# Optimization experiments

Hardware: AMD Instinct MI355X
Metric: run time of the kernel (lower is better)

Reference implementation:

```python
import jax, jax.numpy as jnp
import numpy as np

DIM = 1024
DIM_HEAD = 64
INNER = 1024
HEADS = INNER // DIM_HEAD  # 16
QNUM = 64
MULT = 4
SCALE = DIM_HEAD ** -0.5
EPS = 1e-5


def setup_inputs() -> dict:
    key = jax.random.key(0)
    ks = jax.random.split(key, 9)
    S, B, N = 8, 128, 32
    x = jax.random.normal(ks[0], (S, B, N, DIM), dtype=jnp.float32)
    mask = jax.random.randint(ks[1], (S, B, 1), 0, 2, dtype=jnp.int32)
    q = jax.random.normal(ks[2], (QNUM, INNER), dtype=jnp.float32)
    W_kv = jax.random.normal(ks[3], (DIM, 2 * INNER), dtype=jnp.float32) * 0.02
    ln_g = jnp.ones((INNER,), dtype=jnp.float32)
    ln_b = jnp.zeros((INNER,), dtype=jnp.float32)
    W1 = jax.random.normal(ks[4], (INNER, INNER * MULT * 2), dtype=jnp.float32) * 0.02
    b1 = jnp.zeros((INNER * MULT * 2,), dtype=jnp.float32)
    W2 = jax.random.normal(ks[5], (INNER * MULT, INNER), dtype=jnp.float32) * 0.02
    b2 = jnp.zeros((INNER,), dtype=jnp.float32)
    return {"x": x, "mask": mask, "q": q, "W_kv": W_kv, "ln_g": ln_g,
            "ln_b": ln_b, "W1": W1, "b1": b1, "W2": W2, "b2": b2}


def reference(x, mask, q, W_kv, ln_g, ln_b, W1, b1, W2, b2):
    # x: (S, B, N, D) -> (S, N, B, D); attention keys run over original B axis
    x = jnp.transpose(x, (0, 2, 1, 3))
    S, N, B, _ = x.shape
    kv = x @ W_kv                                  # (S, N, B, 2*INNER)
    k, v = jnp.split(kv, 2, axis=-1)
    # split heads: (S, N, B, I) -> (S, N, H, B, Dh)
    k = k.reshape(S, N, B, HEADS, DIM_HEAD).transpose(0, 1, 3, 2, 4)
    v = v.reshape(S, N, B, HEADS, DIM_HEAD).transpose(0, 1, 3, 2, 4)
    qh = q.reshape(QNUM, HEADS, DIM_HEAD).transpose(1, 0, 2)  # (H, Q, Dh)
    sim = jnp.einsum('hqd,snhjd->snhqj', qh, k) * SCALE        # (S,N,H,Q,B)
    # mask: (S, B, J); rearrange 's i j->s j i' then [:,0,:] == mask[:, :, 0]
    m = mask[:, :, 0][:, None, None, None, :]                  # (S,1,1,1,B)
    sim = jnp.where(m == 0, jnp.float32(-1e10), sim)
    attn = jax.nn.softmax(sim, axis=-1)
    out = jnp.einsum('snhqj,snhjd->snhqd', attn, v)            # (S,N,H,Q,Dh)
    out = out.transpose(0, 1, 3, 2, 4).reshape(S, N, QNUM, INNER)
    # PreNorm(Residual(FeedForward)): y = LN(out); return FF(y) + y
    mu = jnp.mean(out, axis=-1, keepdims=True)
    var = jnp.var(out, axis=-1, keepdims=True)
    y = (out - mu) * jax.lax.rsqrt(var + EPS) * ln_g + ln_b
    u = y @ W1 + b1
    a, g = jnp.split(u, 2, axis=-1)
    ff = (a * jax.nn.gelu(g, approximate=False)) @ W2 + b2
    return ff + y
```

## Files before the change

### kernel.cpp

```cpp
#include <hip/hip_runtime.h>
#include <stdint.h>
#include <math.h>

#define SCALE  0.125f

typedef __bf16 bf16;
typedef __bf16 bf16x8 __attribute__((ext_vector_type(8)));
typedef float  f32x4  __attribute__((ext_vector_type(4)));
typedef float  f32x16 __attribute__((ext_vector_type(16)));

__device__ __forceinline__ ushort f2b(float f) {
  union { float f; uint32_t u; } v; v.f = f;
  uint32_t u = v.u;
  return (ushort)((u + 0x7fffu + ((u >> 16) & 1u)) >> 16);
}
__device__ __forceinline__ float b2f(ushort s) {
  union { uint32_t u; float f; } v; v.u = ((uint32_t)s) << 16;
  return v.f;
}
__device__ __forceinline__ void g2l16(const ushort* g, ushort* l) {
  __builtin_amdgcn_global_load_lds(
      (const __attribute__((address_space(1))) void*)g,
      (__attribute__((address_space(3))) void*)l, 16, 0, 0);
}
__device__ __forceinline__ float erf_fast(float x) {
  float ax = fabsf(x);
  float t  = __builtin_amdgcn_rcpf(1.0f + 0.3275911f * ax);
  float p  = t * (0.254829592f + t * (-0.284496736f + t * (1.421413741f +
             t * (-1.453152027f + t * 1.061405429f))));
  float e  = __expf(-ax * ax);
  float r  = 1.0f - p * e;
  return copysignf(r, x);
}

__global__ __launch_bounds__(256) void conv_x_kernel(const float* __restrict__ x,
                                                     ushort* __restrict__ xb) {
  int idx = blockIdx.x * 256 + threadIdx.x;
  int d4 = idx & 255;
  int n  = (idx >> 8) & 31;
  int b  = (idx >> 13) & 127;
  int s  = idx >> 20;
  float4 v = *(const float4*)(x + (size_t)(((s*128 + b)*32 + n) << 10) + (d4 << 2));
  ushort4 o;
  o.x = f2b(v.x); o.y = f2b(v.y); o.z = f2b(v.z); o.w = f2b(v.w);
  *(ushort4*)(xb + (size_t)(((s*32 + n)*128 + b) << 10) + (d4 << 2)) = o;
}

__global__ __launch_bounds__(256) void conv_q_kernel(const float* __restrict__ q,
                                                     ushort* __restrict__ qb) {
  int idx = blockIdx.x * 256 + threadIdx.x;
  float4 v = *(const float4*)(q + (size_t)idx * 4);
  ushort4 o;
  o.x = f2b(v.x); o.y = f2b(v.y); o.z = f2b(v.z); o.w = f2b(v.w);
  *(ushort4*)(qb + (size_t)idx * 4) = o;
}

__global__ __launch_bounds__(256) void transpose_w_kernel(const float* __restrict__ W,
                                                          ushort* __restrict__ Wt,
                                                          int K, int N, int mode) {
  __shared__ float tile[32][33];
  int rt = blockIdx.x, kt = blockIdx.y;
  int r0 = rt * 32;
  int tx = threadIdx.x & 31, ty = threadIdx.x >> 5;
  int src;
  if (mode == 1) {
    int rp = r0 + tx;
    int g6 = rp >> 6, w = rp & 63;
    src = (w < 32) ? (g6*32 + w) : (4096 + g6*32 + (w - 32));
  } else {
    src = r0 + tx;
  }
  for (int i = ty; i < 32; i += 8)
    tile[i][tx] = W[(size_t)(kt*32 + i) * N + src];
  __syncthreads();
  for (int i = ty; i < 32; i += 8)
    Wt[(size_t)(r0 + i) * K + kt*32 + tx] = f2b(tile[tx][i]);
}

template <int EPI, int K, int NCOLS>
__global__ __launch_bounds__(256, 4) void gemm_bt(const ushort* __restrict__ A,
                                                  const ushort* __restrict__ Bt,
                                                  float* __restrict__ outf,
                                                  ushort* __restrict__ outb,
                                                  const float* __restrict__ bias,
                                                  const float* __restrict__ resid) {
  __shared__ ushort As[128 * 64];
  __shared__ ushort Bs[128 * 64];
  constexpr int nBn = NCOLS >> 7;
  const int bm = blockIdx.x / nBn, bn = blockIdx.x % nBn;
  const int t = threadIdx.x;
  const int wave = t >> 6, lane = t & 63;
  const int c32 = lane & 31, hi = lane >> 5;
  const int wm = ((wave >> 1) << 6), wn = ((wave & 1) << 6);
  const int swz = c32 & 7;

  const int srow = wave*8 + (lane >> 3);
  const int skg  = (lane & 7) ^ ((lane >> 3) & 7);
  const ushort* ag = A  + (size_t)(bm*128 + srow) * K + skg*8;
  const ushort* bg = Bt + (size_t)(bn*128 + srow) * K + skg*8;
  ushort* asl = As + wave * 512;
  ushort* bsl = Bs + wave * 512;

  f32x16 acc[2][2] = {};

#pragma unroll 2
  for (int k0 = 0; k0 < K; k0 += 64) {
#pragma unroll
    for (int c = 0; c < 4; c++) {
      g2l16(ag + (size_t)c*32*K + k0, asl + c*2048);
      g2l16(bg + (size_t)c*32*K + k0, bsl + c*2048);
    }
    __syncthreads();
#pragma unroll
    for (int kb = 0; kb < 2; kb++) {
      bf16x8 af[2][2], bfr[2][2];
#pragma unroll
      for (int i = 0; i < 2; i++)
#pragma unroll
        for (int k2 = 0; k2 < 2; k2++) {
          int ks = kb*2 + k2;
          int ps = (2*ks + hi) ^ swz;
          af[i][k2]  = *(const bf16x8*)(As + (wm + i*32 + c32)*64 + ps*8);
          bfr[i][k2] = *(const bf16x8*)(Bs + (wn + i*32 + c32)*64 + ps*8);
        }
#pragma unroll
      for (int k2 = 0; k2 < 2; k2++)
#pragma unroll
        for (int i = 0; i < 2; i++)
#pragma unroll
          for (int j = 0; j < 2; j++)
            acc[i][j] = __builtin_amdgcn_mfma_f32_32x32x16_bf16(af[i][k2], bfr[j][k2], acc[i][j], 0, 0, 0);
    }
    __syncthreads();
  }

  if (EPI == 0) {
#pragma unroll
    for (int i = 0; i < 2; i++)
#pragma unroll
      for (int j = 0; j < 2; j++)
#pragma unroll
        for (int reg = 0; reg < 16; reg++) {
          int row = bm*128 + wm + i*32 + (reg & 3) + 8*(reg >> 2) + 4*hi;
          int col = bn*128 + wn + j*32 + c32;
          outb[(size_t)row * NCOLS + col] = f2b(acc[i][j][reg]);
        }
  } else if (EPI == 1) {
    int hcol = bn*64 + (wave & 1)*32 + c32;
    float ba = bias[hcol];
    float bg2 = bias[4096 + hcol];
#pragma unroll
    for (int i = 0; i < 2; i++)
#pragma unroll
      for (int reg = 0; reg < 16; reg++) {
        float a = acc[i][0][reg] + ba;
        float g = acc[i][1][reg] + bg2;
        float ge = 0.5f * g * (1.0f + erf_fast(g * 0.70710678118654752f));
        int row = bm*128 + wm + i*32 + (reg & 3) + 8*(reg >> 2) + 4*hi;
        outb[(size_t)row * 4096 + hcol] = f2b(a * ge);
      }
  } else {
#pragma unroll
    for (int i = 0; i < 2; i++)
#pragma unroll
      for (int j = 0; j < 2; j++) {
        int col = bn*128 + wn + j*32 + c32;
        float bc = bias[col];
#pragma unroll
        for (int reg = 0; reg < 16; reg++) {
          int row = bm*128 + wm + i*32 + (reg & 3) + 8*(reg >> 2) + 4*hi;
          size_t o = (size_t)row * NCOLS + col;
          outf[o] = acc[i][j][reg] + bc + resid[o];
        }
      }
  }
}

__global__ __launch_bounds__(256) void attn_kernel(const ushort* __restrict__ kv,
                                                   const ushort* __restrict__ qb,
                                                   const int* __restrict__ mask,
                                                   float* __restrict__ out) {
  __shared__ ushort Ks[128 * 72];
  __shared__ ushort Vt[64 * 136];
  __shared__ ushort Ps[64 * 136];
  __shared__ float  Mrow[128];

  const int bid = blockIdx.x;
  const int h = bid & 15, n = (bid >> 4) & 31, s = bid >> 9;
  const size_t kvbase = (size_t)((s*32 + n) * 128) * 2048;
  const int t = threadIdx.x, wave = t >> 6, lane = t & 63;
  const int qq = lane >> 4, r = lane & 15;

  if (t < 128) Mrow[t] = (mask[s*128 + t] == 0) ? 1.0f : 0.0f;

  for (int c = t; c < 1024; c += 256) {
    int b = c >> 3, d0 = (c & 7) * 8;
    uint4 v = *(const uint4*)(kv + kvbase + (size_t)b * 2048 + h*64 + d0);
    *(uint4*)(Ks + b*72 + d0) = v;
  }
  {
    int b = t & 127, dh = t >> 7;
    for (int jj = 0; jj < 32; jj += 8) {
      uint4 v = *(const uint4*)(kv + kvbase + (size_t)b * 2048 + 1024 + h*64 + dh*32 + jj);
      const ushort* pv = (const ushort*)&v;
#pragma unroll
      for (int u8 = 0; u8 < 8; u8++)
        Vt[(dh*32 + jj + u8)*136 + b] = pv[u8];
    }
  }
  __syncthreads();

  bf16x8 aq[2];
#pragma unroll
  for (int st = 0; st < 2; st++)
    aq[st] = *(const bf16x8*)(qb + (size_t)(wave*16 + r) * 1024 + h*64 + st*32 + qq*8);
  f32x4 sim[8];
#pragma unroll
  for (int jt = 0; jt < 8; jt++) {
    f32x4 c = {};
#pragma unroll
    for (int st = 0; st < 2; st++) {
      bf16x8 bk = *(const bf16x8*)(Ks + (jt*16 + r)*72 + st*32 + qq*8);
      c = __builtin_amdgcn_mfma_f32_16x16x32_bf16(aq[st], bk, c, 0, 0, 0);
    }
    sim[jt] = c;
  }

#pragma unroll
  for (int jt = 0; jt < 8; jt++) {
    float mflag = Mrow[jt*16 + r];
#pragma unroll
    for (int ii = 0; ii < 4; ii++) {
      float v = sim[jt][ii] * SCALE;
      sim[jt][ii] = (mflag > 0.5f) ? -1e10f : v;
    }
  }
  float mx[4] = {-3.0e38f, -3.0e38f, -3.0e38f, -3.0e38f};
#pragma unroll
  for (int jt = 0; jt < 8; jt++)
#pragma unroll
    for (int ii = 0; ii < 4; ii++) mx[ii] = fmaxf(mx[ii], sim[jt][ii]);
#pragma unroll
  for (int m = 1; m < 16; m <<= 1)
#pragma unroll
    for (int ii = 0; ii < 4; ii++) mx[ii] = fmaxf(mx[ii], __shfl_xor(mx[ii], m));
  float sm[4] = {0.f, 0.f, 0.f, 0.f};
#pragma unroll
  for (int jt = 0; jt < 8; jt++)
#pragma unroll
    for (int ii = 0; ii < 4; ii++) {
      float e = expf(sim[jt][ii] - mx[ii]);
      sim[jt][ii] = e;
      sm[ii] += e;
    }
#pragma unroll
  for (int m = 1; m < 16; m <<= 1)
#pragma unroll
    for (int ii = 0; ii < 4; ii++) sm[ii] += __shfl_xor(sm[ii], m);
#pragma unroll
  for (int ii = 0; ii < 4; ii++) sm[ii] = 1.0f / sm[ii];
#pragma unroll
  for (int jt = 0; jt < 8; jt++)
#pragma unroll
    for (int ii = 0; ii < 4; ii++)
      Ps[(wave*16 + qq*4 + ii)*136 + jt*16 + r] = f2b(sim[jt][ii] * sm[ii]);
  __syncthreads();

  f32x4 o[4] = {};
#pragma unroll
  for (int kst = 0; kst < 4; kst++) {
    bf16x8 ap = *(const bf16x8*)(Ps + (wave*16 + r)*136 + kst*32 + qq*8);
#pragma unroll
    for (int jt2 = 0; jt2 < 4; jt2++) {
      bf16x8 bv = *(const bf16x8*)(Vt + (jt2*16 + r)*136 + kst*32 + qq*8);
      o[jt2] = __builtin_amdgcn_mfma_f32_16x16x32_bf16(ap, bv, o[jt2], 0, 0, 0);
    }
  }
  const size_t orow0 = (size_t)((s*32 + n) * 64);
#pragma unroll
  for (int jt2 = 0; jt2 < 4; jt2++)
#pragma unroll
    for (int ii = 0; ii < 4; ii++) {
      int qr = wave*16 + qq*4 + ii;
      int d  = jt2*16 + r;
      out[(orow0 + qr) * 1024 + h*64 + d] = o[jt2][ii];
    }
}

__global__ __launch_bounds__(256) void ln_kernel(float* __restrict__ y,
                                                 ushort* __restrict__ yb,
                                                 const float* __restrict__ g,
                                                 const float* __restrict__ b) {
  __shared__ float r1[4], r2[4];
  const int row = blockIdx.x, t = threadIdx.x;
  const int wave = t >> 6, lane = t & 63;
  float* p = y + (size_t)row * 1024;
  float4 v = *(const float4*)(p + t*4);
  float s1 = v.x + v.y + v.z + v.w;
  float s2 = v.x*v.x + v.y*v.y + v.z*v.z + v.w*v.w;
#pragma unroll
  for (int m = 1; m < 64; m <<= 1) { s1 += __shfl_xor(s1, m); s2 += __shfl_xor(s2, m); }
  if (lane == 0) { r1[wave] = s1; r2[wave] = s2; }
  __syncthreads();
  s1 = r1[0] + r1[1] + r1[2] + r1[3];
  s2 = r2[0] + r2[1] + r2[2] + r2[3];
  float mu  = s1 * (1.0f/1024.0f);
  float var = s2 * (1.0f/1024.0f) - mu*mu;
  float inv = rsqrtf(var + 1e-5f);
  float4 gg = *(const float4*)(g + t*4);
  float4 bb = *(const float4*)(b + t*4);
  float4 o;
  o.x = (v.x - mu)*inv*gg.x + bb.x;
  o.y = (v.y - mu)*inv*gg.y + bb.y;
  o.z = (v.z - mu)*inv*gg.z + bb.z;
  o.w = (v.w - mu)*inv*gg.w + bb.w;
  *(float4*)(p + t*4) = o;
  ushort4 ob; ob.x = f2b(o.x); ob.y = f2b(o.y); ob.z = f2b(o.z); ob.w = f2b(o.w);
  *(ushort4*)(yb + (size_t)row * 1024 + t*4) = ob;
}

extern "C" void kernel_launch(void* const* d_in, const int* in_sizes, int n_in,
                              void* d_out, int out_size, void* d_ws, size_t ws_size,
                              hipStream_t stream) {
  const float* x    = (const float*)d_in[0];
  const int*   mask = (const int*)  d_in[1];
  const float* q    = (const float*)d_in[2];
  const float* Wkv  = (const float*)d_in[3];
  const float* lng  = (const float*)d_in[4];
  const float* lnb  = (const float*)d_in[5];
  const float* W1   = (const float*)d_in[6];
  const float* b1   = (const float*)d_in[7];
  const float* W2   = (const float*)d_in[8];
  const float* b2   = (const float*)d_in[9];
  float* out = (float*)d_out;
  char* ws = (char*)d_ws;

  ushort* xb   = (ushort*)(ws);
  float*  yf   = (float*) (ws);
  ushort* kvb  = (ushort*)(ws + 67108864);
  ushort* hid  = (ushort*)(ws + 67108864);
  ushort* yb   = (ushort*)(ws + 201326592);
  ushort* wkvt = (ushort*)(ws + 234881024);
  ushort* w1t  = (ushort*)(ws + 239075328);
  ushort* w2t  = (ushort*)(ws + 255852544);
  ushort* qb   = (ushort*)(ws + 264241152);

  conv_x_kernel<<<32768, 256, 0, stream>>>(x, xb);
  conv_q_kernel<<<64, 256, 0, stream>>>(q, qb);
  transpose_w_kernel<<<dim3(64, 32),  256, 0, stream>>>(Wkv, wkvt, 1024, 2048, 0);
  transpose_w_kernel<<<dim3(256, 32), 256, 0, stream>>>(W1,  w1t,  1024, 8192, 1);
  transpose_w_kernel<<<dim3(32, 128), 256, 0, stream>>>(W2,  w2t,  4096, 1024, 0);

  gemm_bt<0, 1024, 2048><<<4096, 256, 0, stream>>>(xb, wkvt, nullptr, kvb, nullptr, nullptr);
  attn_kernel<<<4096, 256, 0, stream>>>(kvb, qb, mask, yf);
  ln_kernel<<<16384, 256, 0, stream>>>(yf, yb, lng, lnb);
  gemm_bt<1, 1024, 8192><<<8192, 256, 0, stream>>>(yb, w1t, nullptr, hid, b1, nullptr);
  gemm_bt<2, 4096, 1024><<<1024, 256, 0, stream>>>(hid, w2t, out, nullptr, b2, yf);
}
```

Measured before the change: 954.3 us.

## Replace 128x128 GEMM with double-buffered 256x256 tile pipelined kernel

Replaces the single-buffered 128x128-tile GEMM with a 512-thread kernel that computes 256x256 output tiles using 16x16x32 MFMAs. The kernel double-buffers LDS, issues the next K-tile's global-to-LDS loads interleaved with MFMA phases, raises priority during MFMA, and remaps block IDs across 8 groups for cache locality. The larger tile raises arithmetic intensity and the pipeline hides load latency. In exchange it uses 128KB of LDS per block, relies on manual waitcnt and barrier ordering, and leaves fewer blocks per grid, so the small W2 GEMM (256 blocks) may underfill the GPU.

```diff
diff --git a/kernel.cpp b/kernel.cpp
--- a/kernel.cpp
+++ b/kernel.cpp
@@ -7,7 +7,6 @@
 typedef __bf16 bf16;
 typedef __bf16 bf16x8 __attribute__((ext_vector_type(8)));
 typedef float  f32x4  __attribute__((ext_vector_type(4)));
-typedef float  f32x16 __attribute__((ext_vector_type(16)));
 
 __device__ __forceinline__ ushort f2b(float f) {
   union { float f; uint32_t u; } v; v.f = f;
@@ -78,101 +77,177 @@
 }
 
 template <int EPI, int K, int NCOLS>
-__global__ __launch_bounds__(256, 4) void gemm_bt(const ushort* __restrict__ A,
+__global__ __launch_bounds__(512, 2) void gemm256(const ushort* __restrict__ A,
                                                   const ushort* __restrict__ Bt,
                                                   float* __restrict__ outf,
                                                   ushort* __restrict__ outb,
                                                   const float* __restrict__ bias,
                                                   const float* __restrict__ resid) {
-  __shared__ ushort As[128 * 64];
-  __shared__ ushort Bs[128 * 64];
-  constexpr int nBn = NCOLS >> 7;
-  const int bm = blockIdx.x / nBn, bn = blockIdx.x % nBn;
+  __shared__ ushort As[2][16384];
+  __shared__ ushort Bs[2][16384];
+  constexpr int NT  = K / 64;
+  constexpr int nBn = NCOLS / 256;
+
+  const int nwg = (int)gridDim.x;
+  const int bid = (int)blockIdx.x;
+  const int wg  = (bid & 7) * (nwg >> 3) + (bid >> 3);
+  const int bm = wg / nBn, bn = wg % nBn;
+
   const int t = threadIdx.x;
   const int wave = t >> 6, lane = t & 63;
-  const int c32 = lane & 31, hi = lane >> 5;
-  const int wm = ((wave >> 1) << 6), wn = ((wave & 1) << 6);
-  const int swz = c32 & 7;
-
-  const int srow = wave*8 + (lane >> 3);
-  const int skg  = (lane & 7) ^ ((lane >> 3) & 7);
-  const ushort* ag = A  + (size_t)(bm*128 + srow) * K + skg*8;
-  const ushort* bg = Bt + (size_t)(bn*128 + srow) * K + skg*8;
-  ushort* asl = As + wave * 512;
-  ushort* bsl = Bs + wave * 512;
-
-  f32x16 acc[2][2] = {};
-
-#pragma unroll 2
-  for (int k0 = 0; k0 < K; k0 += 64) {
-#pragma unroll
-    for (int c = 0; c < 4; c++) {
-      g2l16(ag + (size_t)c*32*K + k0, asl + c*2048);
-      g2l16(bg + (size_t)c*32*K + k0, bsl + c*2048);
-    }
-    __syncthreads();
-#pragma unroll
-    for (int kb = 0; kb < 2; kb++) {
-      bf16x8 af[2][2], bfr[2][2];
-#pragma unroll
-      for (int i = 0; i < 2; i++)
-#pragma unroll
-        for (int k2 = 0; k2 < 2; k2++) {
-          int ks = kb*2 + k2;
-          int ps = (2*ks + hi) ^ swz;
-          af[i][k2]  = *(const bf16x8*)(As + (wm + i*32 + c32)*64 + ps*8);
-          bfr[i][k2] = *(const bf16x8*)(Bs + (wn + i*32 + c32)*64 + ps*8);
-        }
-#pragma unroll
-      for (int k2 = 0; k2 < 2; k2++)
-#pragma unroll
-        for (int i = 0; i < 2; i++)
-#pragma unroll
-          for (int j = 0; j < 2; j++)
-            acc[i][j] = __builtin_amdgcn_mfma_f32_32x32x16_bf16(af[i][k2], bfr[j][k2], acc[i][j], 0, 0, 0);
-    }
-    __syncthreads();
-  }
+  const int wm = wave >> 2, wn = wave & 3;
+  const int c15 = lane & 15, qq = lane >> 4;
+  const int swz = c15 & 7;
+
+  const int rowc = t >> 3;
+  const int kg = (t & 7) ^ (rowc & 7);
+  const ushort* ag = A  + (size_t)(bm*256 + rowc) * K + kg*8;
+  const ushort* bg = Bt + (size_t)(bn*256 + rowc) * K + kg*8;
+
+  f32x4 acc[8][4] = {};
+
+#define LDA_F(buf, mi, kh) \
+  (*(const bf16x8*)(&As[buf][(wm*128 + (mi)*16 + c15)*64 + ((((kh)*4 + qq) ^ swz)*8)]))
+#define LDB_F(buf, ni, kh) \
+  (*(const bf16x8*)(&Bs[buf][(wn*64 + (ni)*16 + c15)*64 + ((((kh)*4 + qq) ^ swz)*8)]))
+#define STG_A(c, buf, kt) \
+  g2l16(ag + (size_t)(c)*64*K + (size_t)(kt)*64, &As[buf][(c)*4096 + wave*512])
+#define STG_B(c, buf, kt) \
+  g2l16(bg + (size_t)(c)*64*K + (size_t)(kt)*64, &Bs[buf][(c)*4096 + wave*512])
+
+#define MFMA8(p, aa, ab, kh) \
+  _Pragma("unroll") \
+  for (int ni = 0; ni < 4; ++ni) { \
+    acc[2*(p)][ni]   = __builtin_amdgcn_mfma_f32_16x16x32_bf16((aa), bfv[ni][(kh)], acc[2*(p)][ni],   0, 0, 0); \
+    acc[2*(p)+1][ni] = __builtin_amdgcn_mfma_f32_16x16x32_bf16((ab), bfv[ni][(kh)], acc[2*(p)+1][ni], 0, 0, 0); \
+  }
+
+  STG_B(0, 0, 0); STG_B(1, 0, 0); STG_B(2, 0, 0); STG_B(3, 0, 0);
+  STG_A(0, 0, 0); STG_A(2, 0, 0); STG_A(1, 0, 0); STG_A(3, 0, 0);
+  asm volatile("s_waitcnt vmcnt(2)" ::: "memory");
+  __builtin_amdgcn_s_barrier();
+
+#define TILE(kt, cur) { \
+    const int nx_ = (cur) ^ 1; \
+    const int tn_ = ((kt) + 1 == NT) ? 0 : ((kt) + 1); \
+    bf16x8 bfv[4][2]; \
+     { \
+      bf16x8 a00 = LDA_F(cur, 0, 0), a01 = LDA_F(cur, 0, 1); \
+      bf16x8 a10 = LDA_F(cur, 1, 0), a11 = LDA_F(cur, 1, 1); \
+      _Pragma("unroll") \
+      for (int ni = 0; ni < 4; ++ni) { bfv[ni][0] = LDB_F(cur, ni, 0); bfv[ni][1] = LDB_F(cur, ni, 1); } \
+      STG_B(0, nx_, tn_); STG_B(1, nx_, tn_); \
+      __builtin_amdgcn_s_barrier(); \
+      asm volatile("s_waitcnt lgkmcnt(0)" ::: "memory"); \
+      __builtin_amdgcn_sched_barrier(0); \
+      __builtin_amdgcn_s_setprio(1); \
+      MFMA8(0, a00, a10, 0); MFMA8(0, a01, a11, 1); \
+      __builtin_amdgcn_s_setprio(0); \
+      __builtin_amdgcn_s_barrier(); \
+    } \
+     { \
+      bf16x8 a00 = LDA_F(cur, 2, 0), a01 = LDA_F(cur, 2, 1); \
+      bf16x8 a10 = LDA_F(cur, 3, 0), a11 = LDA_F(cur, 3, 1); \
+      STG_B(2, nx_, tn_); STG_B(3, nx_, tn_); \
+      __builtin_amdgcn_s_barrier(); \
+      asm volatile("s_waitcnt lgkmcnt(0)" ::: "memory"); \
+      __builtin_amdgcn_sched_barrier(0); \
+      __builtin_amdgcn_s_setprio(1); \
+      MFMA8(1, a00, a10, 0); MFMA8(1, a01, a11, 1); \
+      __builtin_amdgcn_s_setprio(0); \
+      asm volatile("s_waitcnt vmcnt(4)" ::: "memory"); \
+      __builtin_amdgcn_s_barrier(); \
+    } \
+     { \
+      bf16x8 a00 = LDA_F(cur, 4, 0), a01 = LDA_F(cur, 4, 1); \
+      bf16x8 a10 = LDA_F(cur, 5, 0), a11 = LDA_F(cur, 5, 1); \
+      STG_A(0, nx_, tn_); STG_A(2, nx_, tn_); \
+      __builtin_amdgcn_s_barrier(); \
+      asm volatile("s_waitcnt lgkmcnt(0)" ::: "memory"); \
+      __builtin_amdgcn_sched_barrier(0); \
+      __builtin_amdgcn_s_setprio(1); \
+      MFMA8(2, a00, a10, 0); MFMA8(2, a01, a11, 1); \
+      __builtin_amdgcn_s_setprio(0); \
+      __builtin_amdgcn_s_barrier(); \
+    } \
+     { \
+      bf16x8 a00 = LDA_F(cur, 6, 0), a01 = LDA_F(cur, 6, 1); \
+      bf16x8 a10 = LDA_F(cur, 7, 0), a11 = LDA_F(cur, 7, 1); \
+      STG_A(1, nx_, tn_); STG_A(3, nx_, tn_); \
+      __builtin_amdgcn_s_barrier(); \
+      asm volatile("s_waitcnt lgkmcnt(0)" ::: "memory"); \
+      __builtin_amdgcn_sched_barrier(0); \
+      __builtin_amdgcn_s_setprio(1); \
+      MFMA8(3, a00, a10, 0); MFMA8(3, a01, a11, 1); \
+      __builtin_amdgcn_s_setprio(0); \
+      asm volatile("s_waitcnt vmcnt(2)" ::: "memory"); \
+      __builtin_amdgcn_s_barrier(); \
+    } \
+  }
+
+#pragma unroll 1
+  for (int kt = 0; kt < NT; kt += 2) {
+    TILE(kt, 0);
+    TILE(kt + 1, 1);
+  }
+  asm volatile("s_waitcnt vmcnt(0)" ::: "memory");
+
+#undef TILE
+#undef MFMA8
+#undef STG_A
+#undef STG_B
+#undef LDA_F
+#undef LDB_F
 
   if (EPI == 0) {
 #pragma unroll
-    for (int i = 0; i < 2; i++)
-#pragma unroll
-      for (int j = 0; j < 2; j++)
-#pragma unroll
-        for (int reg = 0; reg < 16; reg++) {
-          int row = bm*128 + wm + i*32 + (reg & 3) + 8*(reg >> 2) + 4*hi;
-          int col = bn*128 + wn + j*32 + c32;
-          outb[(size_t)row * NCOLS + col] = f2b(acc[i][j][reg]);
-        }
-  } else if (EPI == 1) {
-    int hcol = bn*64 + (wave & 1)*32 + c32;
-    float ba = bias[hcol];
-    float bg2 = bias[4096 + hcol];
-#pragma unroll
-    for (int i = 0; i < 2; i++)
-#pragma unroll
-      for (int reg = 0; reg < 16; reg++) {
-        float a = acc[i][0][reg] + ba;
-        float g = acc[i][1][reg] + bg2;
-        float ge = 0.5f * g * (1.0f + erf_fast(g * 0.70710678118654752f));
-        int row = bm*128 + wm + i*32 + (reg & 3) + 8*(reg >> 2) + 4*hi;
-        outb[(size_t)row * 4096 + hcol] = f2b(a * ge);
-      }
-  } else {
-#pragma unroll
-    for (int i = 0; i < 2; i++)
-#pragma unroll
-      for (int j = 0; j < 2; j++) {
-        int col = bn*128 + wn + j*32 + c32;
-        float bc = bias[col];
-#pragma unroll
-        for (int reg = 0; reg < 16; reg++) {
-          int row = bm*128 + wm + i*32 + (reg & 3) + 8*(reg >> 2) + 4*hi;
-          size_t o = (size_t)row * NCOLS + col;
-          outf[o] = acc[i][j][reg] + bc + resid[o];
+    for (int mi = 0; mi < 8; ++mi) {
+      int row0 = bm*256 + wm*128 + mi*16 + qq*4;
+#pragma unroll
+      for (int j = 0; j < 4; ++j) {
+#pragma unroll
+        for (int ni = 0; ni < 4; ++ni) {
+          int col = bn*256 + wn*64 + ni*16 + c15;
+          outb[(size_t)(row0 + j) * NCOLS + col] = f2b(acc[mi][ni][j]);
         }
       }
+    }
+  } else if (EPI == 1) {
+    const int g6 = bn*4 + wn;
+    const int hcol0 = g6*32 + c15;
+    float ba0 = bias[hcol0],        ba1 = bias[hcol0 + 16];
+    float bg0 = bias[4096 + hcol0], bg1 = bias[4096 + hcol0 + 16];
+#pragma unroll
+    for (int mi = 0; mi < 8; ++mi) {
+      int row0 = bm*256 + wm*128 + mi*16 + qq*4;
+#pragma unroll
+      for (int j = 0; j < 4; ++j) {
+        float a0 = acc[mi][0][j] + ba0, g0 = acc[mi][2][j] + bg0;
+        float a1 = acc[mi][1][j] + ba1, g1 = acc[mi][3][j] + bg1;
+        float ge0 = 0.5f * g0 * (1.0f + erf_fast(g0 * 0.70710678118654752f));
+        float ge1 = 0.5f * g1 * (1.0f + erf_fast(g1 * 0.70710678118654752f));
+        size_t rb = (size_t)(row0 + j) * 4096;
+        outb[rb + hcol0]      = f2b(a0 * ge0);
+        outb[rb + hcol0 + 16] = f2b(a1 * ge1);
+      }
+    }
+  } else {
+    float bc[4];
+#pragma unroll
+    for (int ni = 0; ni < 4; ++ni) bc[ni] = bias[bn*256 + wn*64 + ni*16 + c15];
+#pragma unroll
+    for (int mi = 0; mi < 8; ++mi) {
+      int row0 = bm*256 + wm*128 + mi*16 + qq*4;
+#pragma unroll
+      for (int j = 0; j < 4; ++j) {
+#pragma unroll
+        for (int ni = 0; ni < 4; ++ni) {
+          int col = bn*256 + wn*64 + ni*16 + c15;
+          size_t o = (size_t)(row0 + j) * NCOLS + col;
+          outf[o] = acc[mi][ni][j] + bc[ni] + resid[o];
+        }
+      }
+    }
   }
 }
 
@@ -351,9 +426,9 @@
   transpose_w_kernel<<<dim3(256, 32), 256, 0, stream>>>(W1,  w1t,  1024, 8192, 1);
   transpose_w_kernel<<<dim3(32, 128), 256, 0, stream>>>(W2,  w2t,  4096, 1024, 0);
 
-  gemm_bt<0, 1024, 2048><<<4096, 256, 0, stream>>>(xb, wkvt, nullptr, kvb, nullptr, nullptr);
+  gemm256<0, 1024, 2048><<<1024, 512, 0, stream>>>(xb, wkvt, nullptr, kvb, nullptr, nullptr);
   attn_kernel<<<4096, 256, 0, stream>>>(kvb, qb, mask, yf);
   ln_kernel<<<16384, 256, 0, stream>>>(yf, yb, lng, lnb);
-  gemm_bt<1, 1024, 8192><<<8192, 256, 0, stream>>>(yb, w1t, nullptr, hid, b1, nullptr);
-  gemm_bt<2, 4096, 1024><<<1024, 256, 0, stream>>>(hid, w2t, out, nullptr, b2, yf);
-}
+  gemm256<1, 1024, 8192><<<2048, 512, 0, stream>>>(yb, w1t, nullptr, hid, b1, nullptr);
+  gemm256<2, 4096, 1024><<<256, 512, 0, stream>>>(hid, w2t, out, nullptr, b2, yf);
+}
```

Result: faster. 885.1 us (-7.3%).
